# Optimization experiments

Hardware: AMD Instinct MI355X
Metric: run time of the kernel (lower is better)

The kernel has to match this reference:

```python
import jax, jax.numpy as jnp
import numpy as np

B, D, V, S = 256, 784, 128, 2  # batch, dim, max_val, n_steps
ITER_PER_CYCLE = 10
STEP_SIZES = [0.5] + [0.1] * (ITER_PER_CYCLE - 1)   # sbc: [big_step] + [small_step]*...
BAL_CONSTS = [0.9] + [0.6] * (ITER_PER_CYCLE - 1)   # sbc: [big_bal] + [small_bal]*...
TEMP = 1.0


def setup_inputs() -> dict:
    key = jax.random.key(0)
    k1, k2, k3, k4, k5 = jax.random.split(key, 5)
    x = jax.random.randint(k1, (B, D), 0, V, dtype=jnp.int32)
    W = jax.random.normal(k2, (D, D), dtype=jnp.float32) * (1.0 / D)  # keep energies moderate
    b = jax.random.normal(k3, (D,), dtype=jnp.float32) * 0.1
    # Pre-sampled Gumbel noise for the categorical proposal (one slab per inner step)
    ug = jax.random.uniform(k4, (S, B, D, V), dtype=jnp.float32, minval=1e-6, maxval=1.0 - 1e-6)
    gumbel = -jnp.log(-jnp.log(ug))
    # Uniform draws for the MH accept/reject test
    u = jax.random.uniform(k5, (S, B), dtype=jnp.float32)
    k_iter = 0
    return {"x": x, "W": W, "b": b, "gumbel": gumbel, "u": u, "k_iter": k_iter}


def reference(x, W, b, gumbel, u, k_iter):
    step_size = STEP_SIZES[k_iter % ITER_PER_CYCLE]
    bal = BAL_CONSTS[k_iter % ITER_PER_CYCLE]
    Wsym = 0.5 * (W + W.T)

    def model(xf):                      # energy: [B]
        return 0.5 * jnp.einsum('bi,bi->b', xf, xf @ Wsym) + xf @ b

    def gradf(xf):                      # d(energy)/dx: [B, D]
        return xf @ Wsym + b

    disc = jnp.arange(V, dtype=jnp.float32)[None, None, :]  # [1,1,V]

    def calc_logits(xf, g):
        # term1 - term2 from _calc_logits, fused elementwise over [B, D, V]
        diff = disc - xf[:, :, None]
        return g[:, :, None] * diff * bal - diff * diff * (0.5 / step_size)

    def body(x_cur, inp):
        g_noise, ui = inp
        xf = x_cur.astype(jnp.float32)
        g = gradf(xf)
        logits = calc_logits(xf, g)                                  # [B,D,V]
        x_delta = jnp.argmax(logits + g_noise, axis=-1)              # categorical sample [B,D]
        logp = jax.nn.log_softmax(logits, axis=-1)
        lp_forward = jnp.take_along_axis(logp, x_delta[:, :, None], axis=-1)[..., 0].sum(axis=1)
        xdf = x_delta.astype(jnp.float32)
        gd = gradf(xdf) / TEMP
        logits_d = calc_logits(xdf, gd)
        logp_d = jax.nn.log_softmax(logits_d, axis=-1)
        lp_reverse = jnp.take_along_axis(logp_d, x_cur[:, :, None], axis=-1)[..., 0].sum(axis=1)
        la = model(xdf) - model(xf) + lp_reverse - lp_forward        # log accept ratio [B]
        acc = jnp.exp(la) > ui
        x_new = jnp.where(acc[:, None], x_delta, x_cur).astype(x_cur.dtype)
        return x_new, la

    x_out, las = jax.lax.scan(body, x, (gumbel, u))
    return x_out, las[-1]
```

## Files before the change

### kernel.cpp

```cpp
#include <hip/hip_runtime.h>

#define B_ 256
#define D_ 784
#define V_ 128
#define S_ 2
#define BD (B_ * D_)
#define KSPLIT 8
#define KC 98

__device__ __forceinline__ void get_params(const int* kiter, float& ss, float& bal) {
    int k = kiter[0] % 10;
    ss  = (k == 0) ? 0.5f : 0.1f;
    bal = (k == 0) ? 0.9f : 0.6f;
}

__device__ __forceinline__ double wave_red(double v) {
#pragma unroll
    for (int o = 32; o > 0; o >>= 1) v += __shfl_down(v, o, 64);
    return v;
}

__global__ __launch_bounds__(256) void symmetrize_k(
    const float* __restrict__ W, float* __restrict__ Wsym)
{
    __shared__ float tile[32][33];
    const int bx = blockIdx.x * 32, by = blockIdx.y * 32;
    const int tx = threadIdx.x & 31, ty4 = (threadIdx.x >> 5) * 4;
#pragma unroll
    for (int i = 0; i < 4; ++i) {
        int r = by + ty4 + i, c = bx + tx;
        tile[ty4 + i][tx] = (r < D_ && c < D_) ? W[r * D_ + c] : 0.f;
    }
    __syncthreads();
#pragma unroll
    for (int i = 0; i < 4; ++i) {
        int r = bx + ty4 + i, c = by + tx;
        if (r < D_ && c < D_)
            Wsym[r * D_ + c] = 0.5f * (W[r * D_ + c] + tile[tx][ty4 + i]);
    }
}

__global__ __launch_bounds__(256) void gemm_splitk(
    const int* __restrict__ Aint, const float* __restrict__ Wsym,
    float* __restrict__ Cp)
{
    const int bt = blockIdx.x, dt = blockIdx.y, kz = blockIdx.z;
    const int tid = threadIdx.x;
    const int k0 = kz * KC, kend = k0 + KC;

    __shared__ float As[64][20];
    __shared__ float Ws[16][68];

    const int tx = tid & 15, ty = tid >> 4;
    const int arow = tid >> 2, ac0 = (tid & 3) * 4;
    const int wrow = tid >> 4, wc0 = (tid & 15) * 4;
    const int wd0 = dt * 64 + wc0;

    float acc[4][4] = {};

    for (int kb = k0; kb < kend; kb += 16) {
#pragma unroll
        for (int c = 0; c < 4; ++c) {
            int k = kb + ac0 + c;
            As[arow][ac0 + c] = (k < kend) ? (float)Aint[(bt * 64 + arow) * D_ + k] : 0.f;
        }
        {
            int k = kb + wrow;
            float4 wv = (k < kend && wd0 < D_)
                ? *(const float4*)&Wsym[k * D_ + wd0]
                : make_float4(0.f, 0.f, 0.f, 0.f);
            *(float4*)&Ws[wrow][wc0] = wv;
        }
        __syncthreads();
#pragma unroll
        for (int kk = 0; kk < 16; kk += 4) {
            float va[4][4], vw[4][4];
#pragma unroll
            for (int i = 0; i < 4; ++i) {
                float4 t = *(const float4*)&As[ty * 4 + i][kk];
                va[i][0] = t.x; va[i][1] = t.y; va[i][2] = t.z; va[i][3] = t.w;
            }
#pragma unroll
            for (int m = 0; m < 4; ++m) {
                float4 t = *(const float4*)&Ws[kk + m][tx * 4];
                vw[m][0] = t.x; vw[m][1] = t.y; vw[m][2] = t.z; vw[m][3] = t.w;
            }
#pragma unroll
            for (int m = 0; m < 4; ++m)
#pragma unroll
                for (int i = 0; i < 4; ++i)
#pragma unroll
                    for (int j = 0; j < 4; ++j)
                        acc[i][j] = fmaf(va[i][m], vw[m][j], acc[i][j]);
        }
        __syncthreads();
    }

    const int d0 = dt * 64 + tx * 4;
    if (d0 < D_) {
#pragma unroll
        for (int i = 0; i < 4; ++i) {
            int bb = bt * 64 + ty * 4 + i;
            *(float4*)&Cp[(size_t)kz * BD + (size_t)bb * D_ + d0] =
                make_float4(acc[i][0], acc[i][1], acc[i][2], acc[i][3]);
        }
    }
}

__global__ __launch_bounds__(832) void forward_k(
    const int* __restrict__ xin, const float* __restrict__ gpart,
    const float* __restrict__ bvec, const float* __restrict__ gumbel,
    const int* __restrict__ kiter, int s,
    int* __restrict__ x_delta, double* __restrict__ lpf, double* __restrict__ Exf)
{
    const int b = blockIdx.x, tid = threadIdx.x;
    float ss, bal; get_params(kiter, ss, bal);
    const float c2 = 0.5f / ss;

    double lp_acc = 0.0, e_acc = 0.0;

    if (tid < D_) {
        const int d = tid, bd = b * D_ + d;
        const int xi = xin[bd];
        const float xfv = (float)xi;

        float gv = 0.f;
#pragma unroll
        for (int p = 0; p < KSPLIT; ++p) gv += gpart[(size_t)p * BD + bd];
        gv += bvec[d];

        const float a1 = bal * gv;
        const float v0 = xfv + a1 * ss;
        int vm = (int)rintf(v0); vm = min(127, max(0, vm));
        const float dmv = v0 - (float)vm;
        const float Reff = sqrtf(30.0f / c2 + dmv * dmv);
        int lo = max(0, (int)ceilf(v0 - Reff));
        int hi = min(127, (int)floorf(v0 + Reff));
        lo = min(lo, vm); hi = max(hi, vm);

        const float dvm = (float)vm - xfv;
        const float mL = dvm * fmaf(-c2, dvm, a1);

        const float4* __restrict__ gq =
            (const float4*)(gumbel + (((size_t)s * B_ + b) * D_ + d) * V_);
        const int q0 = lo >> 2, qh = hi >> 2;
        float4 quad[4];
#pragma unroll
        for (int j = 0; j < 4; ++j) quad[j] = gq[min(q0 + j, qh)];

        float best = -1e30f; int imax = vm;
        float sum0 = 0.f, sum1 = 0.f;
#pragma unroll
        for (int j = 0; j < 4; ++j) {
            const int qi = q0 + j;
            const bool qok = qi <= qh;
            const float qs[4] = {quad[j].x, quad[j].y, quad[j].z, quad[j].w};
#pragma unroll
            for (int c = 0; c < 4; ++c) {
                int v = 4 * qi + c;
                bool ok = qok && v >= lo && v <= hi;
                float dv = (float)v - xfv;
                float lg = dv * fmaf(-c2, dv, a1);
                float y = ok ? (lg + qs[c]) : -1e30f;
                if (y > best) { best = y; imax = v; }
                float e = expf(lg - mL);
                if (c & 1) sum1 += ok ? e : 0.f; else sum0 += ok ? e : 0.f;
            }
        }
        float lse = mL + logf(sum0 + sum1);
        float dvc = (float)imax - xfv;
        float lch = dvc * fmaf(-c2, dvc, a1);
        lp_acc = (double)(lch - lse);
        e_acc  = (double)xfv * ((double)gv + (double)bvec[d]);
        x_delta[bd] = imax;
    }

    __shared__ double wred[13];
    const int lane = tid & 63, wv = tid >> 6;
    double t = wave_red(lp_acc);
    if (lane == 0) wred[wv] = t;
    __syncthreads();
    if (tid == 0) { double sm = 0; for (int i = 0; i < 13; ++i) sm += wred[i]; lpf[b] = sm; }
    __syncthreads();
    t = wave_red(e_acc);
    if (lane == 0) wred[wv] = t;
    __syncthreads();
    if (tid == 0) { double sm = 0; for (int i = 0; i < 13; ++i) sm += wred[i]; Exf[b] = sm; }
}

__global__ __launch_bounds__(832) void reverse_k(
    const int* __restrict__ xin, int* __restrict__ x_cur,
    const int* __restrict__ x_delta,
    const float* __restrict__ gpart, const float* __restrict__ bvec,
    const float* __restrict__ u, const int* __restrict__ kiter,
    int s, int last, const double* __restrict__ lpf, const double* __restrict__ Exf,
    float* __restrict__ out)
{
    const int b = blockIdx.x, tid = threadIdx.x;
    float ss, bal; get_params(kiter, ss, bal);
    const float c2 = 0.5f / ss;

    double lp_acc = 0.0, e_acc = 0.0;

    if (tid < D_) {
        const int d = tid, bd = b * D_ + d;
        const int xi = xin[bd];
        const int xd = x_delta[bd];
        const float xdv = (float)xd;

        float gv = 0.f;
#pragma unroll
        for (int p = 0; p < KSPLIT; ++p) gv += gpart[(size_t)p * BD + bd];
        gv += bvec[d];

        const float a1 = bal * gv;
        const float v0 = xdv + a1 * ss;
        int vm = (int)rintf(v0); vm = min(127, max(0, vm));
        const float dmv = v0 - (float)vm;
        const float Reff = sqrtf(30.0f / c2 + dmv * dmv);
        int lo = max(0, (int)ceilf(v0 - Reff));
        int hi = min(127, (int)floorf(v0 + Reff));
        lo = min(lo, vm); hi = max(hi, vm);

        const float dvm = (float)vm - xdv;
        const float mL = dvm * fmaf(-c2, dvm, a1);
        float sum0 = 0.f, sum1 = 0.f;
#pragma unroll
        for (int j = 0; j < 16; ++j) {
            int v = lo + j;
            bool ok = v <= hi;
            float dv = (float)v - xdv;
            float lg = dv * fmaf(-c2, dv, a1);
            float e = expf(lg - mL);
            if (j & 1) sum1 += ok ? e : 0.f; else sum0 += ok ? e : 0.f;
        }
        float lse = mL + logf(sum0 + sum1);
        float dvc = (float)xi - xdv;
        float lch = dvc * fmaf(-c2, dvc, a1);
        lp_acc = (double)(lch - lse);
        e_acc  = (double)xdv * ((double)gv + (double)bvec[d]);
    }

    __shared__ double wred[13];
    __shared__ int accept_s;
    __shared__ float la_s;
    const int lane = tid & 63, wv = tid >> 6;

    double t = wave_red(lp_acc);
    if (lane == 0) wred[wv] = t;
    __syncthreads();
    double lpr = 0;
    if (tid == 0) { for (int i = 0; i < 13; ++i) lpr += wred[i]; }
    __syncthreads();
    t = wave_red(e_acc);
    if (lane == 0) wred[wv] = t;
    __syncthreads();
    if (tid == 0) {
        double exd = 0; for (int i = 0; i < 13; ++i) exd += wred[i];
        double la = 0.5 * (exd - Exf[b]) + lpr - lpf[b];
        accept_s = (exp(la) > (double)u[s * B_ + b]) ? 1 : 0;
        la_s = (float)la;
    }
    __syncthreads();

    const int acc = accept_s;
    if (tid < D_) {
        const int bd = b * D_ + tid;
        int xn = acc ? x_delta[bd] : xin[bd];
        x_cur[bd] = xn;
        if (last) out[bd] = (float)xn;
    }
    if (last && tid == 0) out[BD + b] = la_s;
}

extern "C" void kernel_launch(void* const* d_in, const int* in_sizes, int n_in,
                              void* d_out, int out_size, void* d_ws, size_t ws_size,
                              hipStream_t stream)
{
    const int*   x     = (const int*)d_in[0];
    const float* W     = (const float*)d_in[1];
    const float* bv    = (const float*)d_in[2];
    const float* gum   = (const float*)d_in[3];
    const float* u     = (const float*)d_in[4];
    const int*   kiter = (const int*)d_in[5];
    float* out = (float*)d_out;

    char* w = (char*)d_ws;
    size_t off = 0;
    auto carve = [&](size_t bytes) { void* p = w + off; off += (bytes + 511) & ~511ull; return p; };
    int*    x_cur   = (int*)   carve((size_t)BD * 4);
    int*    x_delta = (int*)   carve((size_t)BD * 4);
    float*  gpart   = (float*) carve((size_t)KSPLIT * BD * 4);
    double* lpf     = (double*)carve(B_ * 8);
    double* Exf     = (double*)carve(B_ * 8);
    float*  Wsym    = (float*) carve((size_t)D_ * D_ * 4);
    (void)ws_size; (void)in_sizes; (void)n_in; (void)out_size;

    symmetrize_k<<<dim3(25, 25), 256, 0, stream>>>(W, Wsym);

    for (int s = 0; s < S_; ++s) {
        const int* xin = (s == 0) ? x : x_cur;
        gemm_splitk<<<dim3(4, 13, KSPLIT), 256, 0, stream>>>(xin, Wsym, gpart);
        forward_k<<<B_, 832, 0, stream>>>(xin, gpart, bv, gum, kiter, s,
                                          x_delta, lpf, Exf);
        gemm_splitk<<<dim3(4, 13, KSPLIT), 256, 0, stream>>>(x_delta, Wsym, gpart);
        reverse_k<<<B_, 832, 0, stream>>>(xin, x_cur, x_delta, gpart, bv, u, kiter, s,
                                          (s == S_ - 1) ? 1 : 0, lpf, Exf, out);
    }
}
```

Measured before the change: 349.2 us.

## Fuse split-K GEMM with consumers via atomic counters and reuse step gradient

Each split-K GEMM is merged into the same launch as the kernel that consumes it. GEMM tile blocks publish their partial sums with agent-scope stores and bump a per-row-tile counter. Consumer blocks spin on that counter before reducing the partials. The second step's forward GEMM is dropped by choosing between the saved forward and reverse gradients based on the accept decision. This removes launch gaps and one full GEMM, but relies on spin-waiting inter-block synchronization, which could deadlock if the consumer blocks occupied the GPU before the producer tiles were scheduled.

```diff
diff --git a/kernel.cpp b/kernel.cpp
--- a/kernel.cpp
+++ b/kernel.cpp
@@ -7,6 +7,11 @@
 #define BD (B_ * D_)
 #define KSPLIT 8
 #define KC 98
+#define NJOBS (4 * 13 * KSPLIT)
+#define JOBS_PER_BT (13 * KSPLIT)
+#define NBLK_FUSED (NJOBS + B_)
+#define SUBSZ 2368
+#define AGENT __HIP_MEMORY_SCOPE_AGENT
 
 __device__ __forceinline__ void get_params(const int* kiter, float& ss, float& bal) {
     int k = kiter[0] % 10;
@@ -20,9 +25,87 @@
     return v;
 }
 
+__device__ __forceinline__ float fwd_elem(
+    float xfv, float gv, const float4* __restrict__ gq,
+    float ss, float bal, float c2, int& imax_out)
+{
+    const float a1 = bal * gv;
+    const float v0 = xfv + a1 * ss;
+    int vm = (int)rintf(v0); vm = min(127, max(0, vm));
+    const float dmv = v0 - (float)vm;
+    const float Reff = sqrtf(30.0f / c2 + dmv * dmv);
+    int lo = max(0, (int)ceilf(v0 - Reff));
+    int hi = min(127, (int)floorf(v0 + Reff));
+    lo = min(lo, vm); hi = max(hi, vm);
+
+    const float dvm = (float)vm - xfv;
+    const float mL = dvm * fmaf(-c2, dvm, a1);
+    const int q0 = lo >> 2, qh = hi >> 2;
+    float4 quad[4];
+#pragma unroll
+    for (int j = 0; j < 4; ++j) quad[j] = gq[min(q0 + j, qh)];
+
+    float best = -1e30f; int imax = vm;
+    float sum0 = 0.f, sum1 = 0.f;
+#pragma unroll
+    for (int j = 0; j < 4; ++j) {
+        const int qi = q0 + j;
+        const bool qok = qi <= qh;
+        const float qs[4] = {quad[j].x, quad[j].y, quad[j].z, quad[j].w};
+#pragma unroll
+        for (int c = 0; c < 4; ++c) {
+            int v = 4 * qi + c;
+            bool ok = qok && v >= lo && v <= hi;
+            float dv = (float)v - xfv;
+            float lg = dv * fmaf(-c2, dv, a1);
+            float y = ok ? (lg + qs[c]) : -1e30f;
+            if (y > best) { best = y; imax = v; }
+            float e = expf(lg - mL);
+            if (c & 1) sum1 += ok ? e : 0.f; else sum0 += ok ? e : 0.f;
+        }
+    }
+    float lse = mL + logf(sum0 + sum1);
+    float dvc = (float)imax - xfv;
+    float lch = dvc * fmaf(-c2, dvc, a1);
+    imax_out = imax;
+    return lch - lse;
+}
+
+__device__ __forceinline__ float rev_elem(
+    float xdv, float gv, int xi, float ss, float bal, float c2)
+{
+    const float a1 = bal * gv;
+    const float v0 = xdv + a1 * ss;
+    int vm = (int)rintf(v0); vm = min(127, max(0, vm));
+    const float dmv = v0 - (float)vm;
+    const float Reff = sqrtf(30.0f / c2 + dmv * dmv);
+    int lo = max(0, (int)ceilf(v0 - Reff));
+    int hi = min(127, (int)floorf(v0 + Reff));
+    lo = min(lo, vm); hi = max(hi, vm);
+
+    const float dvm = (float)vm - xdv;
+    const float mL = dvm * fmaf(-c2, dvm, a1);
+    float sum0 = 0.f, sum1 = 0.f;
+#pragma unroll
+    for (int j = 0; j < 16; ++j) {
+        int v = lo + j;
+        bool ok = v <= hi;
+        float dv = (float)v - xdv;
+        float lg = dv * fmaf(-c2, dv, a1);
+        float e = expf(lg - mL);
+        if (j & 1) sum1 += ok ? e : 0.f; else sum0 += ok ? e : 0.f;
+    }
+    float lse = mL + logf(sum0 + sum1);
+    float dvc = (float)xi - xdv;
+    float lch = dvc * fmaf(-c2, dvc, a1);
+    return lch - lse;
+}
+
 __global__ __launch_bounds__(256) void symmetrize_k(
-    const float* __restrict__ W, float* __restrict__ Wsym)
-{
+    const float* __restrict__ W, float* __restrict__ Wsym, int* cnt)
+{
+    if (blockIdx.x == 0 && blockIdx.y == 0 && threadIdx.x < 12)
+        __hip_atomic_store(&cnt[threadIdx.x], 0, __ATOMIC_RELAXED, AGENT);
     __shared__ float tile[32][33];
     const int bx = blockIdx.x * 32, by = blockIdx.y * 32;
     const int tx = threadIdx.x & 31, ty4 = (threadIdx.x >> 5) * 4;
@@ -40,20 +123,16 @@
     }
 }
 
-__global__ __launch_bounds__(256) void gemm_splitk(
-    const int* __restrict__ Aint, const float* __restrict__ Wsym,
-    float* __restrict__ Cp)
-{
-    const int bt = blockIdx.x, dt = blockIdx.y, kz = blockIdx.z;
-    const int tid = threadIdx.x;
+__device__ __forceinline__ void gemm_tile_agent(
+    const int* __restrict__ A, const float* __restrict__ Wsym,
+    float* __restrict__ Cp, float* ldsbuf, int lt, int bt, int dt, int kz)
+{
+    float (*As)[20] = (float(*)[20])ldsbuf;
+    float (*Ws)[68] = (float(*)[68])(ldsbuf + 64 * 20);
     const int k0 = kz * KC, kend = k0 + KC;
-
-    __shared__ float As[64][20];
-    __shared__ float Ws[16][68];
-
-    const int tx = tid & 15, ty = tid >> 4;
-    const int arow = tid >> 2, ac0 = (tid & 3) * 4;
-    const int wrow = tid >> 4, wc0 = (tid & 15) * 4;
+    const int tx = lt & 15, ty = lt >> 4;
+    const int arow = lt >> 2, ac0 = (lt & 3) * 4;
+    const int wrow = lt >> 4, wc0 = (lt & 15) * 4;
     const int wd0 = dt * 64 + wc0;
 
     float acc[4][4] = {};
@@ -62,7 +141,7 @@
 #pragma unroll
         for (int c = 0; c < 4; ++c) {
             int k = kb + ac0 + c;
-            As[arow][ac0 + c] = (k < kend) ? (float)Aint[(bt * 64 + arow) * D_ + k] : 0.f;
+            As[arow][ac0 + c] = (k < kend) ? (float)A[(bt * 64 + arow) * D_ + k] : 0.f;
         }
         {
             int k = kb + wrow;
@@ -101,14 +180,176 @@
 #pragma unroll
         for (int i = 0; i < 4; ++i) {
             int bb = bt * 64 + ty * 4 + i;
-            *(float4*)&Cp[(size_t)kz * BD + (size_t)bb * D_ + d0] =
-                make_float4(acc[i][0], acc[i][1], acc[i][2], acc[i][3]);
-        }
-    }
-}
-
-__global__ __launch_bounds__(832) void forward_k(
-    const int* __restrict__ xin, const float* __restrict__ gpart,
+            size_t base = (size_t)kz * BD + (size_t)bb * D_ + d0;
+#pragma unroll
+            for (int j = 0; j < 4; ++j)
+                __hip_atomic_store(&Cp[base + j], acc[i][j], __ATOMIC_RELAXED, AGENT);
+        }
+    }
+}
+
+__global__ __launch_bounds__(256) void gemm_fwd_fused(
+    const int* __restrict__ xin, const float* __restrict__ Wsym,
+    const float* __restrict__ bvec, const float* __restrict__ gumbel,
+    const int* __restrict__ kiter, int s,
+    float* gpart, int* cnt,
+    int* __restrict__ x_delta, double* __restrict__ lpf,
+    double* __restrict__ Exf, float* __restrict__ gf)
+{
+    const int bid = blockIdx.x, tid = threadIdx.x;
+    float ss, bal; get_params(kiter, ss, bal);
+    const float c2 = 0.5f / ss;
+
+    __shared__ __align__(16) float buf[SUBSZ];
+    __shared__ double wred[4][2];
+
+    if (bid < NJOBS) {
+        const int kz = bid & 7, td = bid >> 3;
+        const int dt = td % 13, bt = td / 13;
+        gemm_tile_agent(xin, Wsym, gpart, buf, tid, bt, dt, kz);
+        __syncthreads();
+        if (tid == 0)
+            __hip_atomic_fetch_add(&cnt[bt], 1, __ATOMIC_RELEASE, AGENT);
+        return;
+    }
+
+    const int b = bid - NJOBS;
+    if (tid == 0) {
+        while (__hip_atomic_load(&cnt[b >> 6], __ATOMIC_ACQUIRE, AGENT) < JOBS_PER_BT)
+            __builtin_amdgcn_s_sleep(2);
+    }
+    __syncthreads();
+
+    double lp_acc = 0.0, e_acc = 0.0;
+#pragma unroll
+    for (int q = 0; q < 4; ++q) {
+        const int d = tid + 256 * q;
+        if (d < D_) {
+            const int bd = b * D_ + d;
+            const float xfv = (float)xin[bd];
+            float gv = 0.f;
+#pragma unroll
+            for (int p = 0; p < KSPLIT; ++p)
+                gv += __hip_atomic_load(&gpart[(size_t)p * BD + bd],
+                                        __ATOMIC_RELAXED, AGENT);
+            const float bvd = bvec[d];
+            gv += bvd;
+            const float4* gq =
+                (const float4*)(gumbel + (((size_t)s * B_ + b) * D_ + d) * V_);
+            int imax;
+            float lp = fwd_elem(xfv, gv, gq, ss, bal, c2, imax);
+            lp_acc += (double)lp;
+            e_acc  += (double)xfv * ((double)gv + (double)bvd);
+            x_delta[bd] = imax;
+            gf[bd] = gv;
+        }
+    }
+    const int lane = tid & 63, wv = tid >> 6;
+    double t = wave_red(lp_acc);
+    if (lane == 0) wred[wv][0] = t;
+    t = wave_red(e_acc);
+    if (lane == 0) wred[wv][1] = t;
+    __syncthreads();
+    if (tid == 0) {
+        double sl = 0, se = 0;
+#pragma unroll
+        for (int i = 0; i < 4; ++i) { sl += wred[i][0]; se += wred[i][1]; }
+        lpf[b] = sl; Exf[b] = se;
+    }
+}
+
+__global__ __launch_bounds__(256) void gemm_rev_fused(
+    const int* __restrict__ xin, int* __restrict__ x_cur,
+    const int* __restrict__ x_delta, const float* __restrict__ Wsym,
+    const float* __restrict__ bvec, const float* __restrict__ u,
+    const int* __restrict__ kiter, int s, int last,
+    float* gpart, int* cnt,
+    const double* __restrict__ lpf, const double* __restrict__ Exf,
+    const float* __restrict__ gf, float* __restrict__ gsel,
+    float* __restrict__ out)
+{
+    const int bid = blockIdx.x, tid = threadIdx.x;
+    float ss, bal; get_params(kiter, ss, bal);
+    const float c2 = 0.5f / ss;
+
+    __shared__ __align__(16) float buf[SUBSZ];
+    __shared__ double wred[4][2];
+    __shared__ int acc_s;
+    __shared__ float la_s;
+
+    if (bid < NJOBS) {
+        const int kz = bid & 7, td = bid >> 3;
+        const int dt = td % 13, bt = td / 13;
+        gemm_tile_agent(x_delta, Wsym, gpart, buf, tid, bt, dt, kz);
+        __syncthreads();
+        if (tid == 0)
+            __hip_atomic_fetch_add(&cnt[bt], 1, __ATOMIC_RELEASE, AGENT);
+        return;
+    }
+
+    const int b = bid - NJOBS;
+    if (tid == 0) {
+        while (__hip_atomic_load(&cnt[b >> 6], __ATOMIC_ACQUIRE, AGENT) < JOBS_PER_BT)
+            __builtin_amdgcn_s_sleep(2);
+    }
+    __syncthreads();
+
+    double lp_acc = 0.0, e_acc = 0.0;
+    float gv_sav[4]; int xi_sav[4], xd_sav[4];
+#pragma unroll
+    for (int q = 0; q < 4; ++q) {
+        const int d = tid + 256 * q;
+        if (d < D_) {
+            const int bd = b * D_ + d;
+            const int xi = xin[bd];
+            const int xd = x_delta[bd];
+            const float xdv = (float)xd;
+            float gv = 0.f;
+#pragma unroll
+            for (int p = 0; p < KSPLIT; ++p)
+                gv += __hip_atomic_load(&gpart[(size_t)p * BD + bd],
+                                        __ATOMIC_RELAXED, AGENT);
+            const float bvd = bvec[d];
+            gv += bvd;
+            gv_sav[q] = gv; xi_sav[q] = xi; xd_sav[q] = xd;
+            float lp = rev_elem(xdv, gv, xi, ss, bal, c2);
+            lp_acc += (double)lp;
+            e_acc  += (double)xdv * ((double)gv + (double)bvd);
+        }
+    }
+    const int lane = tid & 63, wv = tid >> 6;
+    double t = wave_red(lp_acc);
+    if (lane == 0) wred[wv][0] = t;
+    t = wave_red(e_acc);
+    if (lane == 0) wred[wv][1] = t;
+    __syncthreads();
+    if (tid == 0) {
+        double lpr = 0, exd = 0;
+#pragma unroll
+        for (int i = 0; i < 4; ++i) { lpr += wred[i][0]; exd += wred[i][1]; }
+        double la = 0.5 * (exd - Exf[b]) + lpr - lpf[b];
+        acc_s = (exp(la) > (double)u[s * B_ + b]) ? 1 : 0;
+        la_s = (float)la;
+    }
+    __syncthreads();
+
+    const int acc = acc_s;
+#pragma unroll
+    for (int q = 0; q < 4; ++q) {
+        const int d = tid + 256 * q;
+        if (d < D_) {
+            const int bd = b * D_ + d;
+            int xn = acc ? xd_sav[q] : xi_sav[q];
+            x_cur[bd] = xn;
+            if (!last) gsel[bd] = acc ? gv_sav[q] : gf[bd];
+            else       out[bd] = (float)xn;
+        }
+    }
+    if (last && tid == 0) out[BD + b] = la_s;
+}
+
+__global__ __launch_bounds__(832) void forward2_k(
+    const int* __restrict__ xin, const float* __restrict__ gsel,
     const float* __restrict__ bvec, const float* __restrict__ gumbel,
     const int* __restrict__ kiter, int s,
     int* __restrict__ x_delta, double* __restrict__ lpf, double* __restrict__ Exf)
@@ -116,161 +357,32 @@
     const int b = blockIdx.x, tid = threadIdx.x;
     float ss, bal; get_params(kiter, ss, bal);
     const float c2 = 0.5f / ss;
-
     double lp_acc = 0.0, e_acc = 0.0;
-
     if (tid < D_) {
         const int d = tid, bd = b * D_ + d;
-        const int xi = xin[bd];
-        const float xfv = (float)xi;
-
-        float gv = 0.f;
-#pragma unroll
-        for (int p = 0; p < KSPLIT; ++p) gv += gpart[(size_t)p * BD + bd];
-        gv += bvec[d];
-
-        const float a1 = bal * gv;
-        const float v0 = xfv + a1 * ss;
-        int vm = (int)rintf(v0); vm = min(127, max(0, vm));
-        const float dmv = v0 - (float)vm;
-        const float Reff = sqrtf(30.0f / c2 + dmv * dmv);
-        int lo = max(0, (int)ceilf(v0 - Reff));
-        int hi = min(127, (int)floorf(v0 + Reff));
-        lo = min(lo, vm); hi = max(hi, vm);
-
-        const float dvm = (float)vm - xfv;
-        const float mL = dvm * fmaf(-c2, dvm, a1);
-
-        const float4* __restrict__ gq =
+        const float xfv = (float)xin[bd];
+        const float gv = gsel[bd];
+        const float bvd = bvec[d];
+        const float4* gq =
             (const float4*)(gumbel + (((size_t)s * B_ + b) * D_ + d) * V_);
-        const int q0 = lo >> 2, qh = hi >> 2;
-        float4 quad[4];
-#pragma unroll
-        for (int j = 0; j < 4; ++j) quad[j] = gq[min(q0 + j, qh)];
-
-        float best = -1e30f; int imax = vm;
-        float sum0 = 0.f, sum1 = 0.f;
-#pragma unroll
-        for (int j = 0; j < 4; ++j) {
-            const int qi = q0 + j;
-            const bool qok = qi <= qh;
-            const float qs[4] = {quad[j].x, quad[j].y, quad[j].z, quad[j].w};
-#pragma unroll
-            for (int c = 0; c < 4; ++c) {
-                int v = 4 * qi + c;
-                bool ok = qok && v >= lo && v <= hi;
-                float dv = (float)v - xfv;
-                float lg = dv * fmaf(-c2, dv, a1);
-                float y = ok ? (lg + qs[c]) : -1e30f;
-                if (y > best) { best = y; imax = v; }
-                float e = expf(lg - mL);
-                if (c & 1) sum1 += ok ? e : 0.f; else sum0 += ok ? e : 0.f;
-            }
-        }
-        float lse = mL + logf(sum0 + sum1);
-        float dvc = (float)imax - xfv;
-        float lch = dvc * fmaf(-c2, dvc, a1);
-        lp_acc = (double)(lch - lse);
-        e_acc  = (double)xfv * ((double)gv + (double)bvec[d]);
+        int imax;
+        float lp = fwd_elem(xfv, gv, gq, ss, bal, c2, imax);
+        lp_acc = (double)lp;
+        e_acc  = (double)xfv * ((double)gv + (double)bvd);
         x_delta[bd] = imax;
     }
-
-    __shared__ double wred[13];
+    __shared__ double wred[13][2];
     const int lane = tid & 63, wv = tid >> 6;
     double t = wave_red(lp_acc);
-    if (lane == 0) wred[wv] = t;
-    __syncthreads();
-    if (tid == 0) { double sm = 0; for (int i = 0; i < 13; ++i) sm += wred[i]; lpf[b] = sm; }
-    __syncthreads();
+    if (lane == 0) wred[wv][0] = t;
     t = wave_red(e_acc);
-    if (lane == 0) wred[wv] = t;
-    __syncthreads();
-    if (tid == 0) { double sm = 0; for (int i = 0; i < 13; ++i) sm += wred[i]; Exf[b] = sm; }
-}
-
-__global__ __launch_bounds__(832) void reverse_k(
-    const int* __restrict__ xin, int* __restrict__ x_cur,
-    const int* __restrict__ x_delta,
-    const float* __restrict__ gpart, const float* __restrict__ bvec,
-    const float* __restrict__ u, const int* __restrict__ kiter,
-    int s, int last, const double* __restrict__ lpf, const double* __restrict__ Exf,
-    float* __restrict__ out)
-{
-    const int b = blockIdx.x, tid = threadIdx.x;
-    float ss, bal; get_params(kiter, ss, bal);
-    const float c2 = 0.5f / ss;
-
-    double lp_acc = 0.0, e_acc = 0.0;
-
-    if (tid < D_) {
-        const int d = tid, bd = b * D_ + d;
-        const int xi = xin[bd];
-        const int xd = x_delta[bd];
-        const float xdv = (float)xd;
-
-        float gv = 0.f;
-#pragma unroll
-        for (int p = 0; p < KSPLIT; ++p) gv += gpart[(size_t)p * BD + bd];
-        gv += bvec[d];
-
-        const float a1 = bal * gv;
-        const float v0 = xdv + a1 * ss;
-        int vm = (int)rintf(v0); vm = min(127, max(0, vm));
-        const float dmv = v0 - (float)vm;
-        const float Reff = sqrtf(30.0f / c2 + dmv * dmv);
-        int lo = max(0, (int)ceilf(v0 - Reff));
-        int hi = min(127, (int)floorf(v0 + Reff));
-        lo = min(lo, vm); hi = max(hi, vm);
-
-        const float dvm = (float)vm - xdv;
-        const float mL = dvm * fmaf(-c2, dvm, a1);
-        float sum0 = 0.f, sum1 = 0.f;
-#pragma unroll
-        for (int j = 0; j < 16; ++j) {
-            int v = lo + j;
-            bool ok = v <= hi;
-            float dv = (float)v - xdv;
-            float lg = dv * fmaf(-c2, dv, a1);
-            float e = expf(lg - mL);
-            if (j & 1) sum1 += ok ? e : 0.f; else sum0 += ok ? e : 0.f;
-        }
-        float lse = mL + logf(sum0 + sum1);
-        float dvc = (float)xi - xdv;
-        float lch = dvc * fmaf(-c2, dvc, a1);
-        lp_acc = (double)(lch - lse);
-        e_acc  = (double)xdv * ((double)gv + (double)bvec[d]);
-    }
-
-    __shared__ double wred[13];
-    __shared__ int accept_s;
-    __shared__ float la_s;
-    const int lane = tid & 63, wv = tid >> 6;
-
-    double t = wave_red(lp_acc);
-    if (lane == 0) wred[wv] = t;
-    __syncthreads();
-    double lpr = 0;
-    if (tid == 0) { for (int i = 0; i < 13; ++i) lpr += wred[i]; }
-    __syncthreads();
-    t = wave_red(e_acc);
-    if (lane == 0) wred[wv] = t;
+    if (lane == 0) wred[wv][1] = t;
     __syncthreads();
     if (tid == 0) {
-        double exd = 0; for (int i = 0; i < 13; ++i) exd += wred[i];
-        double la = 0.5 * (exd - Exf[b]) + lpr - lpf[b];
-        accept_s = (exp(la) > (double)u[s * B_ + b]) ? 1 : 0;
-        la_s = (float)la;
-    }
-    __syncthreads();
-
-    const int acc = accept_s;
-    if (tid < D_) {
-        const int bd = b * D_ + tid;
-        int xn = acc ? x_delta[bd] : xin[bd];
-        x_cur[bd] = xn;
-        if (last) out[bd] = (float)xn;
-    }
-    if (last && tid == 0) out[BD + b] = la_s;
+        double sl = 0, se = 0;
+        for (int i = 0; i < 13; ++i) { sl += wred[i][0]; se += wred[i][1]; }
+        lpf[b] = sl; Exf[b] = se;
+    }
 }
 
 extern "C" void kernel_launch(void* const* d_in, const int* in_sizes, int n_in,
@@ -291,20 +403,27 @@
     int*    x_cur   = (int*)   carve((size_t)BD * 4);
     int*    x_delta = (int*)   carve((size_t)BD * 4);
     float*  gpart   = (float*) carve((size_t)KSPLIT * BD * 4);
+    float*  Wsym    = (float*) carve((size_t)D_ * D_ * 4);
+    float*  gf      = (float*) carve((size_t)BD * 4);
+    float*  gsel    = (float*) carve((size_t)BD * 4);
     double* lpf     = (double*)carve(B_ * 8);
     double* Exf     = (double*)carve(B_ * 8);
-    float*  Wsym    = (float*) carve((size_t)D_ * D_ * 4);
+    int*    cnt     = (int*)   carve(12 * 4);
     (void)ws_size; (void)in_sizes; (void)n_in; (void)out_size;
 
-    symmetrize_k<<<dim3(25, 25), 256, 0, stream>>>(W, Wsym);
-
-    for (int s = 0; s < S_; ++s) {
-        const int* xin = (s == 0) ? x : x_cur;
-        gemm_splitk<<<dim3(4, 13, KSPLIT), 256, 0, stream>>>(xin, Wsym, gpart);
-        forward_k<<<B_, 832, 0, stream>>>(xin, gpart, bv, gum, kiter, s,
-                                          x_delta, lpf, Exf);
-        gemm_splitk<<<dim3(4, 13, KSPLIT), 256, 0, stream>>>(x_delta, Wsym, gpart);
-        reverse_k<<<B_, 832, 0, stream>>>(xin, x_cur, x_delta, gpart, bv, u, kiter, s,
-                                          (s == S_ - 1) ? 1 : 0, lpf, Exf, out);
-    }
-}
+    symmetrize_k<<<dim3(25, 25), 256, 0, stream>>>(W, Wsym, cnt);
+
+    gemm_fwd_fused<<<NBLK_FUSED, 256, 0, stream>>>(
+        x, Wsym, bv, gum, kiter, 0, gpart, cnt + 0, x_delta, lpf, Exf, gf);
+
+    gemm_rev_fused<<<NBLK_FUSED, 256, 0, stream>>>(
+        x, x_cur, x_delta, Wsym, bv, u, kiter, 0, 0,
+        gpart, cnt + 4, lpf, Exf, gf, gsel, out);
+
+    forward2_k<<<B_, 832, 0, stream>>>(
+        x_cur, gsel, bv, gum, kiter, 1, x_delta, lpf, Exf);
+
+    gemm_rev_fused<<<NBLK_FUSED, 256, 0, stream>>>(
+        x_cur, x_cur, x_delta, Wsym, bv, u, kiter, 1, 1,
+        gpart, cnt + 8, lpf, Exf, gf, gsel, out);
+}
```

Result: slower. 722.1 us (+106.8%).

## Reuse gradient from accepted or rejected state to skip step-two forward GEMM

Applied to the files above, without the earlier changes.

The step-one forward and reverse kernels now save their full gradients (gf for x, gv for x_delta). The reverse kernel selects the gradient matching the accepted state into gsel, so step two's forward pass reads it directly and skips one split-K GEMM plus the partial-sum reduction. This removes one of the four GEMM launches at the cost of extra global writes of B*D floats and a new forward2 kernel.

```diff
diff --git a/kernel.cpp b/kernel.cpp
--- a/kernel.cpp
+++ b/kernel.cpp
@@ -111,7 +111,8 @@
     const int* __restrict__ xin, const float* __restrict__ gpart,
     const float* __restrict__ bvec, const float* __restrict__ gumbel,
     const int* __restrict__ kiter, int s,
-    int* __restrict__ x_delta, double* __restrict__ lpf, double* __restrict__ Exf)
+    int* __restrict__ x_delta, double* __restrict__ lpf, double* __restrict__ Exf,
+    float* __restrict__ gf)
 {
     const int b = blockIdx.x, tid = threadIdx.x;
     float ss, bal; get_params(kiter, ss, bal);
@@ -128,6 +129,7 @@
 #pragma unroll
         for (int p = 0; p < KSPLIT; ++p) gv += gpart[(size_t)p * BD + bd];
         gv += bvec[d];
+        gf[bd] = gv;
 
         const float a1 = bal * gv;
         const float v0 = xfv + a1 * ss;
@@ -188,12 +190,89 @@
     if (tid == 0) { double sm = 0; for (int i = 0; i < 13; ++i) sm += wred[i]; Exf[b] = sm; }
 }
 
+__global__ __launch_bounds__(832) void forward2_k(
+    const int* __restrict__ xin, const float* __restrict__ gsel,
+    const float* __restrict__ bvec, const float* __restrict__ gumbel,
+    const int* __restrict__ kiter, int s,
+    int* __restrict__ x_delta, double* __restrict__ lpf, double* __restrict__ Exf)
+{
+    const int b = blockIdx.x, tid = threadIdx.x;
+    float ss, bal; get_params(kiter, ss, bal);
+    const float c2 = 0.5f / ss;
+
+    double lp_acc = 0.0, e_acc = 0.0;
+
+    if (tid < D_) {
+        const int d = tid, bd = b * D_ + d;
+        const float xfv = (float)xin[bd];
+        const float gv = gsel[bd];
+
+        const float a1 = bal * gv;
+        const float v0 = xfv + a1 * ss;
+        int vm = (int)rintf(v0); vm = min(127, max(0, vm));
+        const float dmv = v0 - (float)vm;
+        const float Reff = sqrtf(30.0f / c2 + dmv * dmv);
+        int lo = max(0, (int)ceilf(v0 - Reff));
+        int hi = min(127, (int)floorf(v0 + Reff));
+        lo = min(lo, vm); hi = max(hi, vm);
+
+        const float dvm = (float)vm - xfv;
+        const float mL = dvm * fmaf(-c2, dvm, a1);
+
+        const float4* __restrict__ gq =
+            (const float4*)(gumbel + (((size_t)s * B_ + b) * D_ + d) * V_);
+        const int q0 = lo >> 2, qh = hi >> 2;
+        float4 quad[4];
+#pragma unroll
+        for (int j = 0; j < 4; ++j) quad[j] = gq[min(q0 + j, qh)];
+
+        float best = -1e30f; int imax = vm;
+        float sum0 = 0.f, sum1 = 0.f;
+#pragma unroll
+        for (int j = 0; j < 4; ++j) {
+            const int qi = q0 + j;
+            const bool qok = qi <= qh;
+            const float qs[4] = {quad[j].x, quad[j].y, quad[j].z, quad[j].w};
+#pragma unroll
+            for (int c = 0; c < 4; ++c) {
+                int v = 4 * qi + c;
+                bool ok = qok && v >= lo && v <= hi;
+                float dv = (float)v - xfv;
+                float lg = dv * fmaf(-c2, dv, a1);
+                float y = ok ? (lg + qs[c]) : -1e30f;
+                if (y > best) { best = y; imax = v; }
+                float e = expf(lg - mL);
+                if (c & 1) sum1 += ok ? e : 0.f; else sum0 += ok ? e : 0.f;
+            }
+        }
+        float lse = mL + logf(sum0 + sum1);
+        float dvc = (float)imax - xfv;
+        float lch = dvc * fmaf(-c2, dvc, a1);
+        lp_acc = (double)(lch - lse);
+        e_acc  = (double)xfv * ((double)gv + (double)bvec[d]);
+        x_delta[bd] = imax;
+    }
+
+    __shared__ double wred[13];
+    const int lane = tid & 63, wv = tid >> 6;
+    double t = wave_red(lp_acc);
+    if (lane == 0) wred[wv] = t;
+    __syncthreads();
+    if (tid == 0) { double sm = 0; for (int i = 0; i < 13; ++i) sm += wred[i]; lpf[b] = sm; }
+    __syncthreads();
+    t = wave_red(e_acc);
+    if (lane == 0) wred[wv] = t;
+    __syncthreads();
+    if (tid == 0) { double sm = 0; for (int i = 0; i < 13; ++i) sm += wred[i]; Exf[b] = sm; }
+}
+
 __global__ __launch_bounds__(832) void reverse_k(
     const int* __restrict__ xin, int* __restrict__ x_cur,
     const int* __restrict__ x_delta,
     const float* __restrict__ gpart, const float* __restrict__ bvec,
     const float* __restrict__ u, const int* __restrict__ kiter,
     int s, int last, const double* __restrict__ lpf, const double* __restrict__ Exf,
+    const float* __restrict__ gf, float* __restrict__ gsel,
     float* __restrict__ out)
 {
     const int b = blockIdx.x, tid = threadIdx.x;
@@ -201,17 +280,21 @@
     const float c2 = 0.5f / ss;
 
     double lp_acc = 0.0, e_acc = 0.0;
+    float gv_sav = 0.f;
+    int xi_sav = 0, xd_sav = 0;
 
     if (tid < D_) {
         const int d = tid, bd = b * D_ + d;
         const int xi = xin[bd];
         const int xd = x_delta[bd];
         const float xdv = (float)xd;
+        xi_sav = xi; xd_sav = xd;
 
         float gv = 0.f;
 #pragma unroll
         for (int p = 0; p < KSPLIT; ++p) gv += gpart[(size_t)p * BD + bd];
         gv += bvec[d];
+        gv_sav = gv;
 
         const float a1 = bal * gv;
         const float v0 = xdv + a1 * ss;
@@ -266,9 +349,10 @@
     const int acc = accept_s;
     if (tid < D_) {
         const int bd = b * D_ + tid;
-        int xn = acc ? x_delta[bd] : xin[bd];
+        int xn = acc ? xd_sav : xi_sav;
         x_cur[bd] = xn;
-        if (last) out[bd] = (float)xn;
+        if (!last) gsel[bd] = acc ? gv_sav : gf[bd];
+        else       out[bd] = (float)xn;
     }
     if (last && tid == 0) out[BD + b] = la_s;
 }
@@ -291,20 +375,23 @@
     int*    x_cur   = (int*)   carve((size_t)BD * 4);
     int*    x_delta = (int*)   carve((size_t)BD * 4);
     float*  gpart   = (float*) carve((size_t)KSPLIT * BD * 4);
+    float*  Wsym    = (float*) carve((size_t)D_ * D_ * 4);
+    float*  gf      = (float*) carve((size_t)BD * 4);
+    float*  gsel    = (float*) carve((size_t)BD * 4);
     double* lpf     = (double*)carve(B_ * 8);
     double* Exf     = (double*)carve(B_ * 8);
-    float*  Wsym    = (float*) carve((size_t)D_ * D_ * 4);
     (void)ws_size; (void)in_sizes; (void)n_in; (void)out_size;
 
     symmetrize_k<<<dim3(25, 25), 256, 0, stream>>>(W, Wsym);
 
-    for (int s = 0; s < S_; ++s) {
-        const int* xin = (s == 0) ? x : x_cur;
-        gemm_splitk<<<dim3(4, 13, KSPLIT), 256, 0, stream>>>(xin, Wsym, gpart);
-        forward_k<<<B_, 832, 0, stream>>>(xin, gpart, bv, gum, kiter, s,
-                                          x_delta, lpf, Exf);
-        gemm_splitk<<<dim3(4, 13, KSPLIT), 256, 0, stream>>>(x_delta, Wsym, gpart);
-        reverse_k<<<B_, 832, 0, stream>>>(xin, x_cur, x_delta, gpart, bv, u, kiter, s,
-                                          (s == S_ - 1) ? 1 : 0, lpf, Exf, out);
-    }
-}
+    gemm_splitk<<<dim3(4, 13, KSPLIT), 256, 0, stream>>>(x, Wsym, gpart);
+    forward_k<<<B_, 832, 0, stream>>>(x, gpart, bv, gum, kiter, 0, x_delta, lpf, Exf, gf);
+    gemm_splitk<<<dim3(4, 13, KSPLIT), 256, 0, stream>>>(x_delta, Wsym, gpart);
+    reverse_k<<<B_, 832, 0, stream>>>(x, x_cur, x_delta, gpart, bv, u, kiter, 0, 0,
+                                      lpf, Exf, gf, gsel, out);
+
+    forward2_k<<<B_, 832, 0, stream>>>(x_cur, gsel, bv, gum, kiter, 1, x_delta, lpf, Exf);
+    gemm_splitk<<<dim3(4, 13, KSPLIT), 256, 0, stream>>>(x_delta, Wsym, gpart);
+    reverse_k<<<B_, 832, 0, stream>>>(x_cur, x_cur, x_delta, gpart, bv, u, kiter, 1, 1,
+                                      lpf, Exf, gf, gsel, out);
+}
```

Measured after the change: 334.3 us. 1.04x faster.
